# Kernel optimization log

Measured on AMD Instinct MI355X. Metric: run time of the kernel, lower is better.

Reference implementation:

```python
import jax, jax.numpy as jnp
import numpy as np

D, N, L = 1024, 128, 128
B, S = 4, 4096

def setup_inputs() -> dict:
    key = jax.random.key(0)
    kx, kq, kk, kv = jax.random.split(key, 4)
    x = jax.random.normal(kx, (B, S, D), dtype=jnp.float32)
    # nn.Linear(d, n, bias=False) weight has shape [n, d]; y = x @ W.T
    Wq = jax.random.normal(kq, (N, D), dtype=jnp.float32) * (1.0 / np.sqrt(D))
    Wk = jax.random.normal(kk, (N, D), dtype=jnp.float32) * (1.0 / np.sqrt(D))
    Wv = jax.random.normal(kv, (L, D), dtype=jnp.float32) * (1.0 / np.sqrt(D))
    return {"x": x, "Wq": Wq, "Wk": Wk, "Wv": Wv}

def reference(x, Wq, Wk, Wv):
    scale = jnp.sqrt(jnp.asarray(D, dtype=x.dtype))  # self.d = sqrt(d) in source
    q = jnp.einsum('bsd,nd->bsn', x, Wq)  # [B,S,N]
    k = jnp.einsum('bsd,nd->bsn', x, Wk)  # [B,S,N]
    v = jnp.einsum('bsd,ld->bsl', x, Wv)  # [B,S,L]
    scores = jnp.einsum('bqn,bkn->bqk', q, k) / scale  # [B,S,S]
    a = jax.nn.softmax(scores, axis=-1)
    return jnp.einsum('bqk,bkl->bql', a, v)  # [B,S,L]
```

## Files before the change

kernel.cpp:

```cpp
#include <hip/hip_runtime.h>
#include <stdint.h>

typedef __attribute__((ext_vector_type(8))) _Float16 f16x8;
typedef __attribute__((ext_vector_type(4))) float f32x4;
typedef __attribute__((ext_vector_type(2))) float f32x2;

#define S_ 4096
#define D_ 1024
#define NROWS 16384
#define QSCALE 0.045084220f
#define EXP2(x) __builtin_amdgcn_exp2f(x)

__global__ __launch_bounds__(256) void cvtw(
    const float* __restrict__ Wq, const float* __restrict__ Wk,
    const float* __restrict__ Wv, _Float16* __restrict__ Wh)
{
  int i = (blockIdx.x * 256 + threadIdx.x) * 8;
  const float* src = (i < 131072) ? Wq : ((i < 262144) ? Wk : Wv);
  int off = i & 131071;
  f32x4 a = *(const f32x4*)(src + off);
  f32x4 b = *(const f32x4*)(src + off + 4);
  f16x8 h;
  #pragma unroll
  for (int j = 0; j < 4; ++j) { h[j] = (_Float16)a[j]; h[j + 4] = (_Float16)b[j]; }
  *(f16x8*)(Wh + i) = h;
}

__global__ __launch_bounds__(256) void gemm_qkv(
    const float* __restrict__ x, const _Float16* __restrict__ Wh,
    _Float16* __restrict__ qk, _Float16* __restrict__ vt)
{
  __shared__ char smem[32768];
  char* Ab[2] = { smem,        smem + 16384 };
  char* Bb[2] = { smem + 8192, smem + 24576 };
  const int tid  = threadIdx.x;
  const int lane = tid & 63, wid = tid >> 6;
  const int g = lane >> 4, l15 = lane & 15;
  const int m0 = blockIdx.x * 64;
  const int by = blockIdx.y;

  const char* pA[2];
  #pragma unroll
  for (int it = 0; it < 2; ++it) {
    int G = it * 256 + tid, row = G >> 3, gg = (G & 7) ^ (row & 7);
    pA[it] = (const char*)x + (size_t)(m0 + row) * 4096 + gg * 16;
  }
  const char* pB[2];
  #pragma unroll
  for (int it = 0; it < 2; ++it) {
    int d = it * 256 + tid;
    int rowhi = d >> 4, tt = (d & 15) ^ (rowhi & 15);
    int row = rowhi * 4 + (tt >> 2), gg = tt & 3;
    pB[it] = (const char*)(Wh + (size_t)by * 131072 + (size_t)row * 1024) + gg * 16;
  }

#define GSTAGE(bi) do {                                                        \
    _Pragma("unroll")                                                          \
    for (int it_ = 0; it_ < 2; ++it_) {                                        \
      __builtin_amdgcn_global_load_lds(pA[it_],                                \
          Ab[bi] + it_ * 4096 + wid * 1024, 16, 0, 0);                         \
      pA[it_] += 128;                                                          \
      __builtin_amdgcn_global_load_lds(pB[it_],                                \
          Bb[bi] + it_ * 4096 + wid * 1024, 16, 0, 0);                         \
      pB[it_] += 64;                                                           \
    }                                                                          \
  } while (0)

  f32x4 acc[4][2] = {};

#define GCOMPUTE(bi) do {                                                      \
    f16x8 af[4], bg[2];                                                        \
    _Pragma("unroll")                                                          \
    for (int mt = 0; mt < 4; ++mt) {                                           \
      int row = mt * 16 + l15;                                                 \
      const char* base = Ab[bi] + row * 128;                                   \
      f32x4 a0 = *(const f32x4*)(base + (((2 * g    ) ^ (row & 7)) << 4));     \
      f32x4 a1 = *(const f32x4*)(base + (((2 * g + 1) ^ (row & 7)) << 4));     \
      _Pragma("unroll")                                                        \
      for (int i = 0; i < 4; ++i) {                                            \
        af[mt][i] = (_Float16)a0[i]; af[mt][i + 4] = (_Float16)a1[i];          \
      }                                                                        \
    }                                                                          \
    _Pragma("unroll")                                                          \
    for (int nt = 0; nt < 2; ++nt) {                                           \
      int row = wid * 32 + nt * 16 + l15;                                      \
      int byte = ((row >> 2) * 256) +                                          \
                 (((((row & 3) << 2) | g) ^ ((row >> 2) & 15)) << 4);          \
      bg[nt] = *(const f16x8*)(Bb[bi] + byte);                                 \
    }                                                                          \
    __builtin_amdgcn_s_setprio(1);                                             \
    _Pragma("unroll")                                                          \
    for (int mt = 0; mt < 4; ++mt)                                             \
      _Pragma("unroll")                                                        \
      for (int nt = 0; nt < 2; ++nt)                                           \
        acc[mt][nt] = __builtin_amdgcn_mfma_f32_16x16x32_f16(af[mt], bg[nt],   \
                                                             acc[mt][nt], 0, 0, 0); \
    __builtin_amdgcn_s_setprio(0);                                             \
  } while (0)

  GSTAGE(0);
  __syncthreads();
  for (int t = 0; t < 32; t += 2) {
    GSTAGE(1);
    GCOMPUTE(0);
    __syncthreads();
    if (t + 2 < 32) GSTAGE(0);
    GCOMPUTE(1);
    __syncthreads();
  }

  if (by < 2) {
    const float sc = (by == 0) ? QSCALE : 1.0f;
    #pragma unroll
    for (int mt = 0; mt < 4; ++mt)
      #pragma unroll
      for (int nt = 0; nt < 2; ++nt)
        #pragma unroll
        for (int r = 0; r < 4; ++r) {
          int row = m0 + mt * 16 + (g << 2) + r;
          int col = by * 128 + wid * 32 + nt * 16 + l15;
          qk[(size_t)row * 256 + col] = (_Float16)(acc[mt][nt][r] * sc);
        }
  } else {
    _Float16* T = (_Float16*)smem;
    #pragma unroll
    for (int mt = 0; mt < 4; ++mt)
      #pragma unroll
      for (int nt = 0; nt < 2; ++nt)
        #pragma unroll
        for (int r = 0; r < 4; ++r)
          T[(mt * 16 + (g << 2) + r) * 128 + wid * 32 + nt * 16 + l15] =
              (_Float16)acc[mt][nt][r];
    __syncthreads();
    const int b = m0 >> 12, s_base = m0 & 4095;
    #pragma unroll
    for (int it = 0; it < 4; ++it) {
      int Wn = it * 256 + tid;
      int f = Wn >> 3, gran = Wn & 7;
      int kk = gran >> 2, q = gran & 3;
      f16x8 v;
      #pragma unroll
      for (int i = 0; i < 8; ++i) {
        int h = i >> 2, j = i & 3;
        v[i] = T[(kk * 32 + h * 16 + q * 4 + j) * 128 + f];
      }
      *(f16x8*)((char*)vt + (size_t)(b * 128 + f) * 8192 + s_base * 2 + gran * 16) = v;
    }
  }
#undef GSTAGE
#undef GCOMPUTE
}

__global__ __launch_bounds__(512, 4) void attn(const _Float16* __restrict__ qk,
                                               const _Float16* __restrict__ vt,
                                               _Float16* __restrict__ pO,
                                               float* __restrict__ pml,
                                               int ntiles)
{
  __shared__ _Float16 K0l[64 * 128], K1l[64 * 128];
  __shared__ _Float16 V0l[64 * 128], V1l[64 * 128];
  const int tid  = threadIdx.x;
  const int lane = tid & 63, wid = tid >> 6;
  const int g = lane >> 4, l15 = lane & 15;
  const int b  = blockIdx.y;
  const int q0 = blockIdx.x * 128;
  const int split = blockIdx.z;
  const int kv_begin = split * (ntiles * 64);

  f16x8 qf[4];
  {
    const size_t qrow = (size_t)(b * S_ + q0 + wid * 16 + l15) * 256;
    #pragma unroll
    for (int kk = 0; kk < 4; ++kk)
      qf[kk] = *(const f16x8*)(qk + qrow + kk * 32 + g * 8);
  }

  const char* gK[2]; const char* gV[2];
  #pragma unroll
  for (int it = 0; it < 2; ++it) {
    int G = it * 512 + tid;
    int row = G >> 4, ch = G & 15;
    gK[it] = (const char*)qk + (size_t)(b * S_ + kv_begin + row) * 512 + 256 +
             (((ch << 4)) ^ ((row & 15) << 4));
    int f = G >> 3, c = G & 7;
    gV[it] = (const char*)vt + (size_t)(b * 128 + f) * 8192 + (kv_begin >> 6) * 128 +
             ((c ^ (f & 7)) << 4);
  }

#define STAGE(Kb, Vb) do {                                                          \
    _Pragma("unroll")                                                               \
    for (int it_ = 0; it_ < 2; ++it_) {                                             \
      __builtin_amdgcn_global_load_lds(gK[it_],                                     \
          (char*)(Kb) + (it_ * 512 + wid * 64) * 16, 16, 0, 0);                     \
      __builtin_amdgcn_global_load_lds(gV[it_],                                     \
          (char*)(Vb) + (it_ * 512 + wid * 64) * 16, 16, 0, 0);                     \
    }                                                                               \
    gK[0] += 32768; gK[1] += 32768; gV[0] += 128; gV[1] += 128;                     \
  } while (0)

  f32x4 oacc[8] = {};
  float m_run = -1e30f, l_run = 0.f;

#define COMPUTE(Kb, Vb) do {                                                        \
    f32x4 sacc[4] = {};                                                             \
    __builtin_amdgcn_s_setprio(1);                                                  \
    _Pragma("unroll")                                                               \
    for (int kk = 0; kk < 4; ++kk) {                                                \
      const char* kb = (const char*)(Kb) + l15 * 256 +                              \
                       (((kk << 6) | (g << 4)) ^ (l15 << 4));                       \
      _Pragma("unroll")                                                             \
      for (int kvt = 0; kvt < 4; ++kvt) {                                           \
        f16x8 kf = *(const f16x8*)(kb + kvt * 4096);                                \
        sacc[kvt] = __builtin_amdgcn_mfma_f32_16x16x32_f16(kf, qf[kk], sacc[kvt],   \
                                                           0, 0, 0);                \
      }                                                                             \
    }                                                                               \
    __builtin_amdgcn_s_setprio(0);                                                  \
    float x0 = fmaxf(fmaxf(sacc[0][0], sacc[0][1]), fmaxf(sacc[0][2], sacc[0][3])); \
    float x1 = fmaxf(fmaxf(sacc[1][0], sacc[1][1]), fmaxf(sacc[1][2], sacc[1][3])); \
    float x2 = fmaxf(fmaxf(sacc[2][0], sacc[2][1]), fmaxf(sacc[2][2], sacc[2][3])); \
    float x3 = fmaxf(fmaxf(sacc[3][0], sacc[3][1]), fmaxf(sacc[3][2], sacc[3][3])); \
    float pmax = fmaxf(fmaxf(x0, x1), fmaxf(x2, x3));                               \
    pmax = fmaxf(pmax, __shfl_xor(pmax, 16));                                       \
    pmax = fmaxf(pmax, __shfl_xor(pmax, 32));                                       \
    if (!__all(pmax - m_run <= 8.0f)) {                                             \
      float m_new = fmaxf(m_run, pmax);                                             \
      float corr  = EXP2(m_run - m_new);                                            \
      l_run *= corr;                                                                \
      m_run  = m_new;                                                               \
      _Pragma("unroll")                                                             \
      for (int r = 0; r < 4; ++r) {                                                 \
        float cr = __builtin_bit_cast(float,                                        \
            __builtin_amdgcn_ds_bpermute((((g << 2) + r) << 2),                     \
                                         __builtin_bit_cast(int, corr)));           \
        _Pragma("unroll")                                                           \
        for (int ft = 0; ft < 8; ++ft) oacc[ft][r] *= cr;                           \
      }                                                                             \
    }                                                                               \
    float psum = 0.f;                                                               \
    f16x8 pa[2];                                                                    \
    _Pragma("unroll")                                                               \
    for (int k2 = 0; k2 < 2; ++k2)                                                  \
      _Pragma("unroll")                                                             \
      for (int i = 0; i < 8; ++i) {                                                 \
        float p = EXP2(sacc[2 * k2 + (i >> 2)][i & 3] - m_run);                     \
        psum += p;                                                                  \
        pa[k2][i] = (_Float16)p;                                                    \
      }                                                                             \
    psum += __shfl_xor(psum, 16);                                                   \
    psum += __shfl_xor(psum, 32);                                                   \
    l_run += psum;                                                                  \
    __builtin_amdgcn_s_setprio(1);                                                  \
    _Pragma("unroll")                                                               \
    for (int k2 = 0; k2 < 2; ++k2) {                                                \
      const char* vb = (const char*)(Vb) + l15 * 128 +                              \
                       (((k2 << 6) | (g << 4)) ^ ((l15 & 7) << 4));                 \
      _Pragma("unroll")                                                             \
      for (int ft = 0; ft < 8; ++ft) {                                              \
        f16x8 vf = *(const f16x8*)(vb + ft * 2048);                                 \
        oacc[ft] = __builtin_amdgcn_mfma_f32_16x16x32_f16(pa[k2], vf, oacc[ft],     \
                                                          0, 0, 0);                 \
      }                                                                             \
    }                                                                               \
    __builtin_amdgcn_s_setprio(0);                                                  \
  } while (0)

  STAGE(K0l, V0l);
  __syncthreads();
  for (int t = 0; t < ntiles; t += 2) {
    STAGE(K1l, V1l);
    COMPUTE(K0l, V0l);
    __syncthreads();
    if (t + 2 < ntiles) STAGE(K0l, V0l);
    COMPUTE(K1l, V1l);
    __syncthreads();
  }

  #pragma unroll
  for (int r = 0; r < 4; ++r) {
    float mr = __builtin_bit_cast(float,
                 __builtin_amdgcn_ds_bpermute((((g << 2) + r) << 2),
                                              __builtin_bit_cast(int, m_run)));
    float lr = __builtin_bit_cast(float,
                 __builtin_amdgcn_ds_bpermute((((g << 2) + r) << 2),
                                              __builtin_bit_cast(int, l_run)));
    float inv = 1.f / lr;
    const int grow = b * S_ + q0 + wid * 16 + (g << 2) + r;
    _Float16* od = pO + ((size_t)split * NROWS + grow) * 128;
    #pragma unroll
    for (int ft = 0; ft < 8; ++ft)
      od[ft * 16 + l15] = (_Float16)(oacc[ft][r] * inv);
    if (l15 == 0)
      *(f32x2*)(pml + ((size_t)split * NROWS + grow) * 2) = f32x2{mr, lr};
  }
#undef STAGE
#undef COMPUTE
}

__global__ __launch_bounds__(256) void combine(const _Float16* __restrict__ pO,
                                               const float* __restrict__ pml,
                                               float* __restrict__ out,
                                               int nsplit)
{
  const int tid  = threadIdx.x;
  const int row  = blockIdx.x * 16 + (tid >> 4);
  const int colg = (tid & 15) * 8;

  float M = -1e30f;
  for (int s = 0; s < nsplit; ++s)
    M = fmaxf(M, pml[((size_t)s * NROWS + row) * 2]);
  float den = 0.f;
  float num[8] = {};
  for (int s = 0; s < nsplit; ++s) {
    f32x2 ml = *(const f32x2*)(pml + ((size_t)s * NROWS + row) * 2);
    float w = EXP2(ml.x - M) * ml.y;
    den += w;
    f16x8 o = *(const f16x8*)(pO + ((size_t)s * NROWS + row) * 128 + colg);
    #pragma unroll
    for (int j = 0; j < 8; ++j) num[j] += w * (float)o[j];
  }
  float inv = 1.f / den;
  f32x4 o0, o1;
  #pragma unroll
  for (int j = 0; j < 4; ++j) { o0[j] = num[j] * inv; o1[j] = num[4 + j] * inv; }
  *(f32x4*)(out + (size_t)row * 128 + colg)     = o0;
  *(f32x4*)(out + (size_t)row * 128 + colg + 4) = o1;
}

extern "C" void kernel_launch(void* const* d_in, const int* in_sizes, int n_in,
                              void* d_out, int out_size, void* d_ws, size_t ws_size,
                              hipStream_t stream)
{
  (void)in_sizes; (void)n_in; (void)out_size;
  const float* x  = (const float*)d_in[0];
  const float* Wq = (const float*)d_in[1];
  const float* Wk = (const float*)d_in[2];
  const float* Wv = (const float*)d_in[3];

  char* ws = (char*)d_ws;
  _Float16* qkbuf = (_Float16*)ws;
  _Float16* vtbuf = (_Float16*)(ws + (size_t)NROWS * 256 * 2);
  const size_t base  = (size_t)NROWS * 256 * 2 + (size_t)4 * 128 * 4096 * 2;
  const size_t perO  = (size_t)NROWS * 128 * 2;
  const size_t perML = (size_t)NROWS * 2 * 4;

  int nsplit = 4;
  while (nsplit > 1 && base + (size_t)nsplit * (perO + perML) > ws_size) nsplit >>= 1;

  _Float16* Whb = (_Float16*)(ws + base);
  _Float16* pO  = (_Float16*)(ws + base);
  float*    pml = (float*)(ws + base + (size_t)nsplit * perO);
  float*    out = (float*)d_out;

  cvtw<<<192, 256, 0, stream>>>(Wq, Wk, Wv, Whb);
  dim3 gg(256, 3);
  gemm_qkv<<<gg, 256, 0, stream>>>(x, Whb, qkbuf, vtbuf);
  dim3 ga(S_ / 128, 4, nsplit);
  attn<<<ga, 512, 0, stream>>>(qkbuf, vtbuf, pO, pml, 64 / nsplit);
  combine<<<NROWS / 16, 256, 0, stream>>>(pO, pml, out, nsplit);
}
```

Measured before the change: 84.05 us.

## Give each attention wave two 16-row query tiles, halving waves per block

The attention kernel now runs 4 waves of 256 threads per block instead of 8. Each wave handles 32 query rows as two 16-row sub-tiles, so every K and V fragment read from LDS feeds two MFMAs. This cuts LDS read traffic per FLOP and gives more independent MFMA chains per wave. In exchange the accumulator and register footprint doubles (launch bounds change to 256,2), which lowers occupancy and raises the risk of spills. Each thread also issues twice as many async global-to-LDS loads per stage.

```diff
diff --git a/kernel.cpp b/kernel.cpp
--- a/kernel.cpp
+++ b/kernel.cpp
@@ -151,7 +151,7 @@
 #undef GCOMPUTE
 }
 
-__global__ __launch_bounds__(512, 4) void attn(const _Float16* __restrict__ qk,
+__global__ __launch_bounds__(256, 2) void attn(const _Float16* __restrict__ qk,
                                                const _Float16* __restrict__ vt,
                                                _Float16* __restrict__ pO,
                                                float* __restrict__ pml,
@@ -167,18 +167,20 @@
   const int split = blockIdx.z;
   const int kv_begin = split * (ntiles * 64);
 
-  f16x8 qf[4];
+  f16x8 qf0[4], qf1[4];
   {
-    const size_t qrow = (size_t)(b * S_ + q0 + wid * 16 + l15) * 256;
-    #pragma unroll
-    for (int kk = 0; kk < 4; ++kk)
-      qf[kk] = *(const f16x8*)(qk + qrow + kk * 32 + g * 8);
-  }
-
-  const char* gK[2]; const char* gV[2];
-  #pragma unroll
-  for (int it = 0; it < 2; ++it) {
-    int G = it * 512 + tid;
+    const size_t qr0 = (size_t)(b * S_ + q0 + wid * 32 + l15) * 256;
+    #pragma unroll
+    for (int kk = 0; kk < 4; ++kk) {
+      qf0[kk] = *(const f16x8*)(qk + qr0 + kk * 32 + g * 8);
+      qf1[kk] = *(const f16x8*)(qk + qr0 + 16 * 256 + kk * 32 + g * 8);
+    }
+  }
+
+  const char* gK[4]; const char* gV[4];
+  #pragma unroll
+  for (int it = 0; it < 4; ++it) {
+    int G = it * 256 + tid;
     int row = G >> 4, ch = G & 15;
     gK[it] = (const char*)qk + (size_t)(b * S_ + kv_begin + row) * 512 + 256 +
              (((ch << 4)) ^ ((row & 15) << 4));
@@ -189,20 +191,20 @@
 
 #define STAGE(Kb, Vb) do {                                                          \
     _Pragma("unroll")                                                               \
-    for (int it_ = 0; it_ < 2; ++it_) {                                             \
+    for (int it_ = 0; it_ < 4; ++it_) {                                             \
       __builtin_amdgcn_global_load_lds(gK[it_],                                     \
-          (char*)(Kb) + (it_ * 512 + wid * 64) * 16, 16, 0, 0);                     \
+          (char*)(Kb) + (it_ * 256 + wid * 64) * 16, 16, 0, 0);                     \
       __builtin_amdgcn_global_load_lds(gV[it_],                                     \
-          (char*)(Vb) + (it_ * 512 + wid * 64) * 16, 16, 0, 0);                     \
+          (char*)(Vb) + (it_ * 256 + wid * 64) * 16, 16, 0, 0);                     \
+      gK[it_] += 32768; gV[it_] += 128;                                             \
     }                                                                               \
-    gK[0] += 32768; gK[1] += 32768; gV[0] += 128; gV[1] += 128;                     \
   } while (0)
 
-  f32x4 oacc[8] = {};
-  float m_run = -1e30f, l_run = 0.f;
+  f32x4 oa0[8] = {}, oa1[8] = {};
+  float m0r = -1e30f, l0r = 0.f, m1r = -1e30f, l1r = 0.f;
 
 #define COMPUTE(Kb, Vb) do {                                                        \
-    f32x4 sacc[4] = {};                                                             \
+    f32x4 s0[4] = {}, s1[4] = {};                                                   \
     __builtin_amdgcn_s_setprio(1);                                                  \
     _Pragma("unroll")                                                               \
     for (int kk = 0; kk < 4; ++kk) {                                                \
@@ -211,45 +213,56 @@
       _Pragma("unroll")                                                             \
       for (int kvt = 0; kvt < 4; ++kvt) {                                           \
         f16x8 kf = *(const f16x8*)(kb + kvt * 4096);                                \
-        sacc[kvt] = __builtin_amdgcn_mfma_f32_16x16x32_f16(kf, qf[kk], sacc[kvt],   \
-                                                           0, 0, 0);                \
+        s0[kvt] = __builtin_amdgcn_mfma_f32_16x16x32_f16(kf, qf0[kk], s0[kvt],      \
+                                                         0, 0, 0);                  \
+        s1[kvt] = __builtin_amdgcn_mfma_f32_16x16x32_f16(kf, qf1[kk], s1[kvt],      \
+                                                         0, 0, 0);                  \
       }                                                                             \
     }                                                                               \
     __builtin_amdgcn_s_setprio(0);                                                  \
-    float x0 = fmaxf(fmaxf(sacc[0][0], sacc[0][1]), fmaxf(sacc[0][2], sacc[0][3])); \
-    float x1 = fmaxf(fmaxf(sacc[1][0], sacc[1][1]), fmaxf(sacc[1][2], sacc[1][3])); \
-    float x2 = fmaxf(fmaxf(sacc[2][0], sacc[2][1]), fmaxf(sacc[2][2], sacc[2][3])); \
-    float x3 = fmaxf(fmaxf(sacc[3][0], sacc[3][1]), fmaxf(sacc[3][2], sacc[3][3])); \
-    float pmax = fmaxf(fmaxf(x0, x1), fmaxf(x2, x3));                               \
-    pmax = fmaxf(pmax, __shfl_xor(pmax, 16));                                       \
-    pmax = fmaxf(pmax, __shfl_xor(pmax, 32));                                       \
-    if (!__all(pmax - m_run <= 8.0f)) {                                             \
-      float m_new = fmaxf(m_run, pmax);                                             \
-      float corr  = EXP2(m_run - m_new);                                            \
-      l_run *= corr;                                                                \
-      m_run  = m_new;                                                               \
+    float p0 = fmaxf(                                                               \
+        fmaxf(fmaxf(fmaxf(s0[0][0], s0[0][1]), fmaxf(s0[0][2], s0[0][3])),          \
+              fmaxf(fmaxf(s0[1][0], s0[1][1]), fmaxf(s0[1][2], s0[1][3]))),         \
+        fmaxf(fmaxf(fmaxf(s0[2][0], s0[2][1]), fmaxf(s0[2][2], s0[2][3])),          \
+              fmaxf(fmaxf(s0[3][0], s0[3][1]), fmaxf(s0[3][2], s0[3][3]))));        \
+    float p1 = fmaxf(                                                               \
+        fmaxf(fmaxf(fmaxf(s1[0][0], s1[0][1]), fmaxf(s1[0][2], s1[0][3])),          \
+              fmaxf(fmaxf(s1[1][0], s1[1][1]), fmaxf(s1[1][2], s1[1][3]))),         \
+        fmaxf(fmaxf(fmaxf(s1[2][0], s1[2][1]), fmaxf(s1[2][2], s1[2][3])),          \
+              fmaxf(fmaxf(s1[3][0], s1[3][1]), fmaxf(s1[3][2], s1[3][3]))));        \
+    p0 = fmaxf(p0, __shfl_xor(p0, 16)); p0 = fmaxf(p0, __shfl_xor(p0, 32));         \
+    p1 = fmaxf(p1, __shfl_xor(p1, 16)); p1 = fmaxf(p1, __shfl_xor(p1, 32));         \
+    if (!__all((p0 - m0r <= 8.0f) && (p1 - m1r <= 8.0f))) {                         \
+      float mn0 = fmaxf(m0r, p0), mn1 = fmaxf(m1r, p1);                             \
+      float c0 = EXP2(m0r - mn0), c1 = EXP2(m1r - mn1);                             \
+      l0r *= c0; m0r = mn0; l1r *= c1; m1r = mn1;                                   \
       _Pragma("unroll")                                                             \
       for (int r = 0; r < 4; ++r) {                                                 \
-        float cr = __builtin_bit_cast(float,                                        \
-            __builtin_amdgcn_ds_bpermute((((g << 2) + r) << 2),                     \
-                                         __builtin_bit_cast(int, corr)));           \
+        int ad = ((g << 2) + r) << 2;                                               \
+        float cr0 = __builtin_bit_cast(float,                                       \
+            __builtin_amdgcn_ds_bpermute(ad, __builtin_bit_cast(int, c0)));         \
+        float cr1 = __builtin_bit_cast(float,                                       \
+            __builtin_amdgcn_ds_bpermute(ad, __builtin_bit_cast(int, c1)));         \
         _Pragma("unroll")                                                           \
-        for (int ft = 0; ft < 8; ++ft) oacc[ft][r] *= cr;                           \
+        for (int ft = 0; ft < 8; ++ft) {                                            \
+          oa0[ft][r] *= cr0; oa1[ft][r] *= cr1;                                     \
+        }                                                                           \
       }                                                                             \
     }                                                                               \
-    float psum = 0.f;                                                               \
-    f16x8 pa[2];                                                                    \
+    float ps0 = 0.f, ps1 = 0.f;                                                     \
+    f16x8 pa0[2], pa1[2];                                                           \
     _Pragma("unroll")                                                               \
     for (int k2 = 0; k2 < 2; ++k2)                                                  \
       _Pragma("unroll")                                                             \
       for (int i = 0; i < 8; ++i) {                                                 \
-        float p = EXP2(sacc[2 * k2 + (i >> 2)][i & 3] - m_run);                     \
-        psum += p;                                                                  \
-        pa[k2][i] = (_Float16)p;                                                    \
+        float e0 = EXP2(s0[2 * k2 + (i >> 2)][i & 3] - m0r);                        \
+        float e1 = EXP2(s1[2 * k2 + (i >> 2)][i & 3] - m1r);                        \
+        ps0 += e0; ps1 += e1;                                                       \
+        pa0[k2][i] = (_Float16)e0; pa1[k2][i] = (_Float16)e1;                       \
       }                                                                             \
-    psum += __shfl_xor(psum, 16);                                                   \
-    psum += __shfl_xor(psum, 32);                                                   \
-    l_run += psum;                                                                  \
+    ps0 += __shfl_xor(ps0, 16); ps0 += __shfl_xor(ps0, 32);                         \
+    ps1 += __shfl_xor(ps1, 16); ps1 += __shfl_xor(ps1, 32);                         \
+    l0r += ps0; l1r += ps1;                                                         \
     __builtin_amdgcn_s_setprio(1);                                                  \
     _Pragma("unroll")                                                               \
     for (int k2 = 0; k2 < 2; ++k2) {                                                \
@@ -258,8 +271,10 @@
       _Pragma("unroll")                                                             \
       for (int ft = 0; ft < 8; ++ft) {                                              \
         f16x8 vf = *(const f16x8*)(vb + ft * 2048);                                 \
-        oacc[ft] = __builtin_amdgcn_mfma_f32_16x16x32_f16(pa[k2], vf, oacc[ft],     \
-                                                          0, 0, 0);                 \
+        oa0[ft] = __builtin_amdgcn_mfma_f32_16x16x32_f16(pa0[k2], vf, oa0[ft],      \
+                                                         0, 0, 0);                  \
+        oa1[ft] = __builtin_amdgcn_mfma_f32_16x16x32_f16(pa1[k2], vf, oa1[ft],      \
+                                                         0, 0, 0);                  \
       }                                                                             \
     }                                                                               \
     __builtin_amdgcn_s_setprio(0);                                                  \
@@ -277,21 +292,25 @@
   }
 
   #pragma unroll
-  for (int r = 0; r < 4; ++r) {
-    float mr = __builtin_bit_cast(float,
-                 __builtin_amdgcn_ds_bpermute((((g << 2) + r) << 2),
-                                              __builtin_bit_cast(int, m_run)));
-    float lr = __builtin_bit_cast(float,
-                 __builtin_amdgcn_ds_bpermute((((g << 2) + r) << 2),
-                                              __builtin_bit_cast(int, l_run)));
-    float inv = 1.f / lr;
-    const int grow = b * S_ + q0 + wid * 16 + (g << 2) + r;
-    _Float16* od = pO + ((size_t)split * NROWS + grow) * 128;
-    #pragma unroll
-    for (int ft = 0; ft < 8; ++ft)
-      od[ft * 16 + l15] = (_Float16)(oacc[ft][r] * inv);
-    if (l15 == 0)
-      *(f32x2*)(pml + ((size_t)split * NROWS + grow) * 2) = f32x2{mr, lr};
+  for (int s = 0; s < 2; ++s) {
+    float mrun = s ? m1r : m0r, lrun = s ? l1r : l0r;
+    f32x4* oa = s ? oa1 : oa0;
+    #pragma unroll
+    for (int r = 0; r < 4; ++r) {
+      int ad = ((g << 2) + r) << 2;
+      float mr = __builtin_bit_cast(float,
+                   __builtin_amdgcn_ds_bpermute(ad, __builtin_bit_cast(int, mrun)));
+      float lr = __builtin_bit_cast(float,
+                   __builtin_amdgcn_ds_bpermute(ad, __builtin_bit_cast(int, lrun)));
+      float inv = 1.f / lr;
+      const int grow = b * S_ + q0 + wid * 32 + s * 16 + (g << 2) + r;
+      _Float16* od = pO + ((size_t)split * NROWS + grow) * 128;
+      #pragma unroll
+      for (int ft = 0; ft < 8; ++ft)
+        od[ft * 16 + l15] = (_Float16)(oa[ft][r] * inv);
+      if (l15 == 0)
+        *(f32x2*)(pml + ((size_t)split * NROWS + grow) * 2) = f32x2{mr, lr};
+    }
   }
 #undef STAGE
 #undef COMPUTE
@@ -356,6 +375,6 @@
   dim3 gg(256, 3);
   gemm_qkv<<<gg, 256, 0, stream>>>(x, Whb, qkbuf, vtbuf);
   dim3 ga(S_ / 128, 4, nsplit);
-  attn<<<ga, 512, 0, stream>>>(qkbuf, vtbuf, pO, pml, 64 / nsplit);
+  attn<<<ga, 256, 0, stream>>>(qkbuf, vtbuf, pO, pml, 64 / nsplit);
   combine<<<NROWS / 16, 256, 0, stream>>>(pO, pml, out, nsplit);
 }
```

After: 83.04 us, median of 3. No clear change (-1.2%).
